# Kernel tuning notes

Hardware: AMD Instinct MI355X
Metric: run time of the kernel (lower is better)

## Reference

```python
import jax, jax.numpy as jnp
import numpy as np

DIM = 1024
HEADS = 16
HEAD_DIM = DIM // HEADS
DECAY = 0.95
EPS = 1e-5


def setup_inputs() -> dict:
    key = jax.random.key(0)
    ks = jax.random.split(key, 11)
    B, S, D = 2, 2048, DIM
    s = 1.0 / np.sqrt(D)
    inp = {
        'x': jax.random.normal(ks[0], (B, S, D), dtype=jnp.float32),
        'Wq': jax.random.normal(ks[1], (D, D), dtype=jnp.float32) * s,
        'bq': jnp.zeros((D,), jnp.float32),
        'Wk': jax.random.normal(ks[2], (D, D), dtype=jnp.float32) * s,
        'bk': jnp.zeros((D,), jnp.float32),
        'Wv': jax.random.normal(ks[3], (D, D), dtype=jnp.float32) * s,
        'bv': jnp.zeros((D,), jnp.float32),
        'Wo': jax.random.normal(ks[4], (D, D), dtype=jnp.float32) * s,
        'bo': jnp.zeros((D,), jnp.float32),
        'gamma': jnp.ones((D,), jnp.float32),
        'beta': jnp.zeros((D,), jnp.float32),
    }
    return inp


def _decay_mask(S, dtype):
    idx = jnp.arange(S)
    diff = (idx[:, None] - idx[None, :]).astype(jnp.float32)
    # decay^(i-j) for i >= j, else 0
    mask = jnp.where(diff >= 0, jnp.exp(diff * np.log(DECAY)), 0.0)
    return mask.astype(dtype)


def reference(x, Wq, bq, Wk, bk, Wv, bv, Wo, bo, gamma, beta):
    B, S, D = x.shape
    H, hd = HEADS, HEAD_DIM

    def split_heads(y):  # [B,S,D] -> [B,H,S,hd]
        return y.reshape(B, S, H, hd).transpose(0, 2, 1, 3)

    q = split_heads(x @ Wq + bq)
    k = split_heads(x @ Wk + bk)
    v = split_heads(x @ Wv + bv)

    mask = _decay_mask(S, x.dtype)  # [S,S]
    scores = jnp.einsum('bhid,bhjd->bhij', q, k) * mask
    out = jnp.einsum('bhij,bhjd->bhid', scores, v)  # [B,H,S,hd]

    out = out.transpose(0, 2, 1, 3).reshape(B, S, D)
    out = out @ Wo + bo

    # GroupNorm(H groups) applied over channel dim with seq as spatial dim
    y = out.transpose(0, 2, 1)            # [B,D,S]
    yg = y.reshape(B, H, hd, S)
    mu = yg.mean(axis=(2, 3), keepdims=True)
    var = yg.var(axis=(2, 3), keepdims=True)
    yn = (yg - mu) / jnp.sqrt(var + EPS)
    yn = yn.reshape(B, D, S) * gamma[None, :, None] + beta[None, :, None]
    return yn.transpose(0, 2, 1)          # [B,S,D]
```

## Files before the change

kernel.cpp:

```cpp
#include <hip/hip_runtime.h>
#include <hip/hip_bf16.h>

typedef unsigned short u16;
typedef __attribute__((ext_vector_type(8))) short short8;
typedef __attribute__((ext_vector_type(4))) float f32x4;
typedef __attribute__((ext_vector_type(4))) unsigned short u16x4;

#define SEQ 2048
#define NH 16
#define HD 64
#define DM 1024
#define LN_DECAY (-0.051293294387550536f)
#define WIN_TILES 4

__device__ __forceinline__ float b2f(u16 u) {
    return __uint_as_float(((unsigned int)u) << 16);
}
__device__ __forceinline__ u16 f2b(float f) {
    unsigned int u = __float_as_uint(f);
    u += 0x7fffu + ((u >> 16) & 1u);
    return (u16)(u >> 16);
}
__device__ __forceinline__ f32x4 mfma16(short8 a, short8 b, f32x4 c) {
    return __builtin_amdgcn_mfma_f32_16x16x32_bf16(a, b, c, 0, 0, 0);
}
__device__ __forceinline__ void gld_lds16(const u16* g, u16* l) {
    __builtin_amdgcn_global_load_lds(
        (const __attribute__((address_space(1))) void*)g,
        (__attribute__((address_space(3))) void*)l, 16, 0, 0);
}

__global__ __launch_bounds__(64) void detect_dtype(const u16* __restrict__ W,
                                                   int* __restrict__ flag) {
    int t = threadIdx.x;
    int hit = 0;
    for (int i = t; i < 512; i += 64) {
        u16 u = W[2 * i];
        int e = (u >> 7) & 0xFF;
        if (e >= 0xC0) hit = 1;
    }
    unsigned long long m = __ballot(hit);
    if (t == 0) *flag = (m != 0ULL) ? 1 : 0;
}

__global__ __launch_bounds__(256) void convert_x(const void* __restrict__ x,
                                                 const int* __restrict__ flag,
                                                 u16* __restrict__ xc) {
    int i = (blockIdx.x * 256 + threadIdx.x) * 4;
    if (*flag) {
        f32x4 v = *(const f32x4*)((const float*)x + i);
        u16x4 o = { f2b(v[0]), f2b(v[1]), f2b(v[2]), f2b(v[3]) };
        *(u16x4*)(xc + i) = o;
    } else {
        *(u16x4*)(xc + i) = *(const u16x4*)((const u16*)x + i);
    }
}

__global__ __launch_bounds__(256) void convert_small(
    const void* __restrict__ p0, const void* __restrict__ p1,
    const void* __restrict__ p2, const void* __restrict__ p3,
    const void* __restrict__ p4, const void* __restrict__ p5,
    const int* __restrict__ flag,
    u16* __restrict__ o0, u16* __restrict__ o1, u16* __restrict__ o2,
    u16* __restrict__ o3, u16* __restrict__ o4, u16* __restrict__ o5) {
    const void* in; u16* out;
    switch (blockIdx.x) {
        case 0: in = p0; out = o0; break;
        case 1: in = p1; out = o1; break;
        case 2: in = p2; out = o2; break;
        case 3: in = p3; out = o3; break;
        case 4: in = p4; out = o4; break;
        default: in = p5; out = o5; break;
    }
    int i = threadIdx.x * 4;
    if (*flag) {
        f32x4 v = *(const f32x4*)((const float*)in + i);
        u16x4 o = { f2b(v[0]), f2b(v[1]), f2b(v[2]), f2b(v[3]) };
        *(u16x4*)(out + i) = o;
    } else {
        *(u16x4*)(out + i) = *(const u16x4*)((const u16*)in + i);
    }
}

__global__ __launch_bounds__(256) void transpose4(
    const void* __restrict__ W0, const void* __restrict__ W1,
    const void* __restrict__ W2, const void* __restrict__ W3,
    const int* __restrict__ flag,
    u16* __restrict__ T0, u16* __restrict__ T1,
    u16* __restrict__ T2, u16* __restrict__ T3)
{
    __shared__ u16 tile[32][33];
    const void* W; u16* T;
    int z = blockIdx.z;
    if (z == 0)      { W = W0; T = T0; }
    else if (z == 1) { W = W1; T = T1; }
    else if (z == 2) { W = W2; T = T2; }
    else             { W = W3; T = T3; }
    int fl = *flag;
    int t = threadIdx.x;
    int r = t >> 5, c = t & 31;
    int bn = blockIdx.x * 32, bk = blockIdx.y * 32;
#pragma unroll
    for (int i = 0; i < 4; i++) {
        size_t idx = (size_t)(bk + r + i*8) * DM + bn + c;
        tile[r + i*8][c] = fl ? f2b(((const float*)W)[idx]) : ((const u16*)W)[idx];
    }
    __syncthreads();
#pragma unroll
    for (int i = 0; i < 4; i++)
        T[(size_t)(bn + r + i*8) * DM + bk + c] = tile[c][r + i*8];
}

__device__ __forceinline__ void gemm_body(
    const u16* __restrict__ A, const u16* __restrict__ BT,
    const u16* __restrict__ bias, u16* __restrict__ outB,
    float* __restrict__ outF, int mode,
    int m0, int n0, int t)
{
    __shared__ u16 As[128*32];
    __shared__ u16 Bs[128*32];
    int w = t >> 6, l = t & 63;
    int lane16 = l & 15, quad = l >> 4;
    int wm = (w >> 1) * 64, wn = (w & 1) * 64;

    int srow   = t >> 2;
    int schunk = (t & 3) ^ ((t >> 3) & 3);

    f32x4 zero = {0.f, 0.f, 0.f, 0.f};
    f32x4 acc[4][4];
#pragma unroll
    for (int i = 0; i < 4; i++)
#pragma unroll
        for (int j = 0; j < 4; j++)
            acc[i][j] = zero;

    const u16* a0 = A  + (size_t)(m0 + srow)      * DM + schunk*8;
    const u16* a1 = A  + (size_t)(m0 + srow + 64) * DM + schunk*8;
    const u16* b0 = BT + (size_t)(n0 + srow)      * DM + schunk*8;
    const u16* b1 = BT + (size_t)(n0 + srow + 64) * DM + schunk*8;

    for (int k0 = 0; k0 < DM; k0 += 32) {
        __syncthreads();
        gld_lds16(a0 + k0, &As[t*8]);
        gld_lds16(a1 + k0, &As[2048 + t*8]);
        gld_lds16(b0 + k0, &Bs[t*8]);
        gld_lds16(b1 + k0, &Bs[2048 + t*8]);
        __syncthreads();
        short8 af[4], bf[4];
#pragma unroll
        for (int i = 0; i < 4; i++) {
            int ra = wm + i*16 + lane16;
            int rb = wn + i*16 + lane16;
            af[i] = *(const short8*)(&As[ra*32 + ((quad ^ ((ra>>1)&3))*8)]);
            bf[i] = *(const short8*)(&Bs[rb*32 + ((quad ^ ((rb>>1)&3))*8)]);
        }
#pragma unroll
        for (int i = 0; i < 4; i++)
#pragma unroll
            for (int j = 0; j < 4; j++)
                acc[i][j] = mfma16(af[i], bf[j], acc[i][j]);
    }

#pragma unroll
    for (int i = 0; i < 4; i++) {
#pragma unroll
        for (int j = 0; j < 4; j++) {
            int n = n0 + wn + j*16 + lane16;
            float bv = b2f(bias[n]);
#pragma unroll
            for (int r = 0; r < 4; r++) {
                int m = m0 + wm + i*16 + quad*4 + r;
                float v = acc[i][j][r] + bv;
                if (mode == 3) {
                    outF[(size_t)m*DM + n] = v;
                } else {
                    int b = m >> 11, s = m & (SEQ-1);
                    int h = n >> 6,  d = n & (HD-1);
                    if (mode == 2)
                        outB[(((size_t)(b*NH + h))*HD + d)*SEQ + s] = f2b(v);
                    else
                        outB[(((size_t)(b*NH + h))*SEQ + s)*HD + d] = f2b(v);
                }
            }
        }
    }
}

__global__ __launch_bounds__(256) void gemm_qkv(
    const u16* __restrict__ x,
    const u16* __restrict__ WqT, const u16* __restrict__ WkT, const u16* __restrict__ WvT,
    const u16* __restrict__ bq, const u16* __restrict__ bk, const u16* __restrict__ bv,
    u16* __restrict__ qb, u16* __restrict__ kb, u16* __restrict__ vTb)
{
    int z = blockIdx.z;
    const u16* BT   = (z==0) ? WqT : (z==1) ? WkT : WvT;
    const u16* bias = (z==0) ? bq  : (z==1) ? bk  : bv;
    u16* outB       = (z==0) ? qb  : (z==1) ? kb  : vTb;
    gemm_body(x, BT, bias, outB, nullptr, (z==2) ? 2 : 0,
              blockIdx.x * 128, blockIdx.y * 128, threadIdx.x);
}

__global__ __launch_bounds__(256) void gemm_out(
    const u16* __restrict__ attn, const u16* __restrict__ WoT,
    const u16* __restrict__ bo, float* __restrict__ proj)
{
    gemm_body(attn, WoT, bo, nullptr, proj, 3,
              blockIdx.x * 128, blockIdx.y * 128, threadIdx.x);
}

__global__ __launch_bounds__(256) void retention(
    const u16* __restrict__ q, const u16* __restrict__ k,
    const u16* __restrict__ vT, u16* __restrict__ attn)
{
    __shared__ u16 Ks[64*64];
    __shared__ u16 Vs[64*64];
    __shared__ u16 Ps[4][16*64];

    int qt = blockIdx.x, bh = blockIdx.y;
    int t = threadIdx.x, w = t >> 6, l = t & 63;
    int c = l & 15, qd = l >> 4;
    int qbase = qt * 64;
    int iwave = qbase + w*16;

    const u16* qh = q  + (size_t)bh * SEQ * HD;
    const u16* kh = k  + (size_t)bh * SEQ * HD;
    const u16* vh = vT + (size_t)bh * HD * SEQ;

    float D[4], E[4];
#pragma unroll
    for (int r = 0; r < 4; r++)
        D[r] = __expf((float)(qd*4 + r) * LN_DECAY);
#pragma unroll
    for (int st = 0; st < 4; st++)
        E[st] = __expf(-(float)(st*16 + c) * LN_DECAY);

    int sr = t >> 3, sc8 = t & 7;

    short8 qf[2];
#pragma unroll
    for (int kk = 0; kk < 2; kk++)
        qf[kk] = *(const short8*)(qh + (size_t)(iwave + c)*HD + kk*32 + qd*8);

    f32x4 zero = {0.f, 0.f, 0.f, 0.f};
    f32x4 oacc[4] = {zero, zero, zero, zero};

    int jt0 = (qt > WIN_TILES) ? (qt - WIN_TILES) : 0;
#pragma unroll 1
    for (int jt = jt0; jt <= qt; jt++) {
        int jbase = jt * 64;
        __syncthreads();
        {
            int r0 = sr, r1 = sr + 32;
            *(short8*)(&Ks[r0*64 + ((sc8 ^ (r0&7))*8)]) = *(const short8*)(kh + (size_t)(jbase+r0)*HD + sc8*8);
            *(short8*)(&Ks[r1*64 + ((sc8 ^ (r1&7))*8)]) = *(const short8*)(kh + (size_t)(jbase+r1)*HD + sc8*8);
            *(short8*)(&Vs[r0*64 + ((sc8 ^ (r0&7))*8)]) = *(const short8*)(vh + (size_t)r0*SEQ + jbase + sc8*8);
            *(short8*)(&Vs[r1*64 + ((sc8 ^ (r1&7))*8)]) = *(const short8*)(vh + (size_t)(r1)*SEQ + jbase + sc8*8);
        }
        __syncthreads();

        f32x4 sacc[4] = {zero, zero, zero, zero};
#pragma unroll
        for (int kk = 0; kk < 2; kk++) {
#pragma unroll
            for (int st = 0; st < 4; st++) {
                int row = st*16 + c;
                short8 bf = *(const short8*)(&Ks[row*64 + (((kk*4+qd) ^ (row&7))*8)]);
                sacc[st] = mfma16(qf[kk], bf, sacc[st]);
            }
        }

        float base = __expf((float)(iwave - jbase) * LN_DECAY);
#pragma unroll
        for (int st = 0; st < 4; st++) {
            int j = jbase + st*16 + c;
            float bE = base * E[st];
#pragma unroll
            for (int r = 0; r < 4; r++) {
                int i = iwave + qd*4 + r;
                float val = (i >= j) ? sacc[st][r] * (bE * D[r]) : 0.0f;
                int row = qd*4 + r;
                int col = st*16 + c;
                Ps[w][row*64 + (((col>>3) ^ (row&7))*8) + (col&7)] = f2b(val);
            }
        }
        asm volatile("s_waitcnt lgkmcnt(0)" ::: "memory");
        short8 pf[2];
#pragma unroll
        for (int kk = 0; kk < 2; kk++)
            pf[kk] = *(const short8*)(&Ps[w][c*64 + (((kk*4+qd) ^ (c&7))*8)]);

#pragma unroll
        for (int kk = 0; kk < 2; kk++) {
#pragma unroll
            for (int nt = 0; nt < 4; nt++) {
                int row = nt*16 + c;
                short8 vf = *(const short8*)(&Vs[row*64 + (((kk*4+qd) ^ (row&7))*8)]);
                oacc[nt] = mfma16(pf[kk], vf, oacc[nt]);
            }
        }
    }

    int b = bh >> 4, h = bh & (NH-1);
#pragma unroll
    for (int nt = 0; nt < 4; nt++) {
        int d = h*HD + nt*16 + c;
#pragma unroll
        for (int r = 0; r < 4; r++) {
            int s = iwave + qd*4 + r;
            attn[((size_t)(b*SEQ + s))*DM + d] = f2b(oacc[nt][r]);
        }
    }
}

__global__ __launch_bounds__(256) void gn_partial(
    const float* __restrict__ proj, float* __restrict__ partials)
{
    int bg = blockIdx.x;
    int chunk = blockIdx.y;
    int b = bg >> 4, g = bg & (NH-1);
    const float* base = proj + (size_t)b*SEQ*DM + g*HD;
    int tid = threadIdx.x;
    int rlane = tid & 15;
    int rrow  = tid >> 4;
    float s = 0.f, ss = 0.f;
#pragma unroll
    for (int it = 0; it < 8; it++) {
        int srow = chunk*128 + it*16 + rrow;
        f32x4 v = *(const f32x4*)(base + (size_t)srow*DM + rlane*4);
        s  += v[0] + v[1] + v[2] + v[3];
        ss += v[0]*v[0] + v[1]*v[1] + v[2]*v[2] + v[3]*v[3];
    }
#pragma unroll
    for (int off = 32; off > 0; off >>= 1) {
        s  += __shfl_down(s, off);
        ss += __shfl_down(ss, off);
    }
    __shared__ float red[8];
    int w = tid >> 6, l = tid & 63;
    if (l == 0) { red[w*2] = s; red[w*2+1] = ss; }
    __syncthreads();
    if (tid == 0) {
        float S  = red[0]+red[2]+red[4]+red[6];
        float SS = red[1]+red[3]+red[5]+red[7];
        partials[(bg*16 + chunk)*2]     = S;
        partials[(bg*16 + chunk)*2 + 1] = SS;
    }
}

__global__ __launch_bounds__(64) void gn_finalize(
    const float* __restrict__ partials, float* __restrict__ stats)
{
    int bg = blockIdx.x;
    int l = threadIdx.x;
    float s  = (l < 16) ? partials[(bg*16 + l)*2]     : 0.f;
    float ss = (l < 16) ? partials[(bg*16 + l)*2 + 1] : 0.f;
#pragma unroll
    for (int off = 8; off > 0; off >>= 1) {
        s  += __shfl_down(s, off);
        ss += __shfl_down(ss, off);
    }
    if (l == 0) {
        const float inv = 1.0f / (float)(SEQ*HD);
        float mu = s * inv;
        float var = ss * inv - mu*mu;
        stats[bg*2]   = mu;
        stats[bg*2+1] = rsqrtf(var + 1e-5f);
    }
}

__global__ __launch_bounds__(256) void gn_apply(
    const float* __restrict__ proj, const float* __restrict__ stats,
    const u16* __restrict__ gamma, const u16* __restrict__ beta,
    const int* __restrict__ flag, void* __restrict__ outv)
{
    int idx = blockIdx.x * 256 + threadIdx.x;
    int d = idx & (DM-1);
    int bs = idx >> 10;
    int b = bs >> 11;
    int g = d >> 6;
    float mu   = stats[(b*NH + g)*2];
    float rstd = stats[(b*NH + g)*2 + 1];
    float v = (proj[idx] - mu) * rstd * b2f(gamma[d]) + b2f(beta[d]);
    if (*flag) ((float*)outv)[idx] = v;
    else       ((u16*)outv)[idx]   = f2b(v);
}

extern "C" void kernel_launch(void* const* d_in, const int* in_sizes, int n_in,
                              void* d_out, int out_size, void* d_ws, size_t ws_size,
                              hipStream_t stream) {
    const void* x     = d_in[0];
    const void* Wq    = d_in[1];
    const void* bq    = d_in[2];
    const void* Wk    = d_in[3];
    const void* bk    = d_in[4];
    const void* Wv    = d_in[5];
    const void* bv    = d_in[6];
    const void* Wo    = d_in[7];
    const void* bo    = d_in[8];
    const void* gamma = d_in[9];
    const void* beta  = d_in[10];

    const size_t MB = 1024*1024;
    char* ws = (char*)d_ws;
    int*   flag     = (int*)ws;
    u16*   bqc      = (u16*)(ws + 4096);
    u16*   bkc      = (u16*)(ws + 8192);
    u16*   bvc      = (u16*)(ws + 12288);
    u16*   boc      = (u16*)(ws + 16384);
    u16*   gammac   = (u16*)(ws + 20480);
    u16*   betac    = (u16*)(ws + 24576);
    float* stats    = (float*)(ws + 28672);
    float* partials = (float*)(ws + 32768);
    u16*   xc     = (u16*)(ws + 1*MB);
    u16*   WqT    = (u16*)(ws + 9*MB);
    u16*   WkT    = (u16*)(ws + 11*MB);
    u16*   WvT    = (u16*)(ws + 13*MB);
    u16*   WoT    = (u16*)(ws + 15*MB);
    u16*   qb     = (u16*)(ws + 17*MB);
    u16*   kb     = (u16*)(ws + 25*MB);
    u16*   vTb    = (u16*)(ws + 33*MB);
    u16*   attn   = (u16*)(ws + 41*MB);
    float* proj   = (float*)(ws + 17*MB);

    detect_dtype<<<1, 64, 0, stream>>>((const u16*)Wq, flag);
    convert_x<<<4096, 256, 0, stream>>>(x, flag, xc);
    convert_small<<<6, 256, 0, stream>>>(bq, bk, bv, bo, gamma, beta, flag,
                                         bqc, bkc, bvc, boc, gammac, betac);
    transpose4<<<dim3(32, 32, 4), 256, 0, stream>>>(Wq, Wk, Wv, Wo, flag, WqT, WkT, WvT, WoT);
    gemm_qkv<<<dim3(32, 8, 3), 256, 0, stream>>>(xc, WqT, WkT, WvT, bqc, bkc, bvc, qb, kb, vTb);
    retention<<<dim3(32, 32), 256, 0, stream>>>(qb, kb, vTb, attn);
    gemm_out<<<dim3(32, 8), 256, 0, stream>>>(attn, WoT, boc, proj);
    gn_partial<<<dim3(32, 16), 256, 0, stream>>>(proj, partials);
    gn_finalize<<<32, 64, 0, stream>>>(partials, stats);
    gn_apply<<<(SEQ*DM*2)/256, 256, 0, stream>>>(proj, stats, gammac, betac, flag, d_out);
}
```

Measured before the change: 193.9 us.

## Fuse prep kernels and GroupNorm statistics into GEMM epilogue via atomics

```diff
diff --git a/kernel.cpp b/kernel.cpp
--- a/kernel.cpp
+++ b/kernel.cpp
@@ -29,92 +29,83 @@
         (const __attribute__((address_space(1))) void*)g,
         (__attribute__((address_space(3))) void*)l, 16, 0, 0);
 }
-
-__global__ __launch_bounds__(64) void detect_dtype(const u16* __restrict__ W,
-                                                   int* __restrict__ flag) {
-    int t = threadIdx.x;
+__device__ __forceinline__ int detect_fl(const u16* Wq, int lane) {
     int hit = 0;
-    for (int i = t; i < 512; i += 64) {
-        u16 u = W[2 * i];
-        int e = (u >> 7) & 0xFF;
-        if (e >= 0xC0) hit = 1;
-    }
-    unsigned long long m = __ballot(hit);
-    if (t == 0) *flag = (m != 0ULL) ? 1 : 0;
-}
-
-__global__ __launch_bounds__(256) void convert_x(const void* __restrict__ x,
-                                                 const int* __restrict__ flag,
-                                                 u16* __restrict__ xc) {
-    int i = (blockIdx.x * 256 + threadIdx.x) * 4;
-    if (*flag) {
-        f32x4 v = *(const f32x4*)((const float*)x + i);
-        u16x4 o = { f2b(v[0]), f2b(v[1]), f2b(v[2]), f2b(v[3]) };
-        *(u16x4*)(xc + i) = o;
+#pragma unroll
+    for (int j = 0; j < 4; j++) {
+        u16 u = Wq[2*(lane + 64*j)];
+        if (((u >> 7) & 0xFF) >= 0xC0) hit = 1;
+    }
+    return (__ballot(hit) != 0ULL) ? 1 : 0;
+}
+
+__global__ __launch_bounds__(256) void prep(
+    const void* __restrict__ x,
+    const void* __restrict__ Wq, const void* __restrict__ Wk,
+    const void* __restrict__ Wv, const void* __restrict__ Wo,
+    const void* __restrict__ bq, const void* __restrict__ bk,
+    const void* __restrict__ bv, const void* __restrict__ bo,
+    const void* __restrict__ gamma, const void* __restrict__ beta,
+    u16* __restrict__ xc,
+    u16* __restrict__ WqT, u16* __restrict__ WkT,
+    u16* __restrict__ WvT, u16* __restrict__ WoT,
+    u16* __restrict__ bqc, u16* __restrict__ bkc, u16* __restrict__ bvc,
+    u16* __restrict__ boc, u16* __restrict__ gammac, u16* __restrict__ betac,
+    int* __restrict__ flag, float* __restrict__ statsAcc)
+{
+    __shared__ u16 tileS[32][33];
+    int bid = blockIdx.x, tid = threadIdx.x;
+    int fl = detect_fl((const u16*)Wq, tid & 63);
+
+    if (bid < 4096) {
+        int i = (bid*256 + tid)*4;
+        if (fl) {
+            f32x4 v = *(const f32x4*)((const float*)x + i);
+            u16x4 o = { f2b(v[0]), f2b(v[1]), f2b(v[2]), f2b(v[3]) };
+            *(u16x4*)(xc + i) = o;
+        } else {
+            *(u16x4*)(xc + i) = *(const u16x4*)((const u16*)x + i);
+        }
+    } else if (bid == 4096) {
+        const void* ins[6] = {bq, bk, bv, bo, gamma, beta};
+        u16* outs[6] = {bqc, bkc, bvc, boc, gammac, betac};
+        int i = tid*4;
+#pragma unroll
+        for (int a = 0; a < 6; a++) {
+            if (fl) {
+                f32x4 v = *(const f32x4*)((const float*)ins[a] + i);
+                u16x4 o = { f2b(v[0]), f2b(v[1]), f2b(v[2]), f2b(v[3]) };
+                *(u16x4*)(outs[a] + i) = o;
+            } else {
+                *(u16x4*)(outs[a] + i) = *(const u16x4*)((const u16*)ins[a] + i);
+            }
+        }
+        if (tid == 0) *flag = fl;
+        if (tid < 64) statsAcc[tid] = 0.f;
     } else {
-        *(u16x4*)(xc + i) = *(const u16x4*)((const u16*)x + i);
-    }
-}
-
-__global__ __launch_bounds__(256) void convert_small(
-    const void* __restrict__ p0, const void* __restrict__ p1,
-    const void* __restrict__ p2, const void* __restrict__ p3,
-    const void* __restrict__ p4, const void* __restrict__ p5,
-    const int* __restrict__ flag,
-    u16* __restrict__ o0, u16* __restrict__ o1, u16* __restrict__ o2,
-    u16* __restrict__ o3, u16* __restrict__ o4, u16* __restrict__ o5) {
-    const void* in; u16* out;
-    switch (blockIdx.x) {
-        case 0: in = p0; out = o0; break;
-        case 1: in = p1; out = o1; break;
-        case 2: in = p2; out = o2; break;
-        case 3: in = p3; out = o3; break;
-        case 4: in = p4; out = o4; break;
-        default: in = p5; out = o5; break;
-    }
-    int i = threadIdx.x * 4;
-    if (*flag) {
-        f32x4 v = *(const f32x4*)((const float*)in + i);
-        u16x4 o = { f2b(v[0]), f2b(v[1]), f2b(v[2]), f2b(v[3]) };
-        *(u16x4*)(out + i) = o;
-    } else {
-        *(u16x4*)(out + i) = *(const u16x4*)((const u16*)in + i);
-    }
-}
-
-__global__ __launch_bounds__(256) void transpose4(
-    const void* __restrict__ W0, const void* __restrict__ W1,
-    const void* __restrict__ W2, const void* __restrict__ W3,
-    const int* __restrict__ flag,
-    u16* __restrict__ T0, u16* __restrict__ T1,
-    u16* __restrict__ T2, u16* __restrict__ T3)
-{
-    __shared__ u16 tile[32][33];
-    const void* W; u16* T;
-    int z = blockIdx.z;
-    if (z == 0)      { W = W0; T = T0; }
-    else if (z == 1) { W = W1; T = T1; }
-    else if (z == 2) { W = W2; T = T2; }
-    else             { W = W3; T = T3; }
-    int fl = *flag;
-    int t = threadIdx.x;
-    int r = t >> 5, c = t & 31;
-    int bn = blockIdx.x * 32, bk = blockIdx.y * 32;
-#pragma unroll
-    for (int i = 0; i < 4; i++) {
-        size_t idx = (size_t)(bk + r + i*8) * DM + bn + c;
-        tile[r + i*8][c] = fl ? f2b(((const float*)W)[idx]) : ((const u16*)W)[idx];
-    }
-    __syncthreads();
-#pragma unroll
-    for (int i = 0; i < 4; i++)
-        T[(size_t)(bn + r + i*8) * DM + bk + c] = tile[c][r + i*8];
-}
-
+        int tb = bid - 4097;
+        int wsel = tb >> 10, tile = tb & 1023;
+        const void* W = (wsel==0) ? Wq : (wsel==1) ? Wk : (wsel==2) ? Wv : Wo;
+        u16* T        = (wsel==0) ? WqT : (wsel==1) ? WkT : (wsel==2) ? WvT : WoT;
+        int bn = (tile & 31)*32, bk_ = (tile >> 5)*32;
+        int r = tid >> 5, c = tid & 31;
+#pragma unroll
+        for (int i2 = 0; i2 < 4; i2++) {
+            size_t idx = (size_t)(bk_ + r + i2*8)*DM + bn + c;
+            tileS[r + i2*8][c] = fl ? f2b(((const float*)W)[idx]) : ((const u16*)W)[idx];
+        }
+        __syncthreads();
+#pragma unroll
+        for (int i2 = 0; i2 < 4; i2++)
+            T[(size_t)(bn + r + i2*8)*DM + bk_ + c] = tileS[c][r + i2*8];
+    }
+}
+
+template<int MODE>
 __device__ __forceinline__ void gemm_body(
     const u16* __restrict__ A, const u16* __restrict__ BT,
     const u16* __restrict__ bias, u16* __restrict__ outB,
-    float* __restrict__ outF, int mode,
+    float* __restrict__ outF, float* __restrict__ stats,
     int m0, int n0, int t)
 {
     __shared__ u16 As[128*32];
@@ -161,6 +152,7 @@
                 acc[i][j] = mfma16(af[i], bf[j], acc[i][j]);
     }
 
+    float s = 0.f, ss = 0.f;
 #pragma unroll
     for (int i = 0; i < 4; i++) {
 #pragma unroll
@@ -171,17 +163,31 @@
             for (int r = 0; r < 4; r++) {
                 int m = m0 + wm + i*16 + quad*4 + r;
                 float v = acc[i][j][r] + bv;
-                if (mode == 3) {
+                if (MODE == 3) {
                     outF[(size_t)m*DM + n] = v;
+                    s += v; ss += v*v;
                 } else {
-                    int b = m >> 11, s = m & (SEQ-1);
+                    int b = m >> 11, sq = m & (SEQ-1);
                     int h = n >> 6,  d = n & (HD-1);
-                    if (mode == 2)
-                        outB[(((size_t)(b*NH + h))*HD + d)*SEQ + s] = f2b(v);
+                    if (MODE == 2)
+                        outB[(((size_t)(b*NH + h))*HD + d)*SEQ + sq] = f2b(v);
                     else
-                        outB[(((size_t)(b*NH + h))*SEQ + s)*HD + d] = f2b(v);
+                        outB[(((size_t)(b*NH + h))*SEQ + sq)*HD + d] = f2b(v);
                 }
             }
+        }
+    }
+    if (MODE == 3) {
+#pragma unroll
+        for (int off = 32; off > 0; off >>= 1) {
+            s  += __shfl_down(s, off);
+            ss += __shfl_down(ss, off);
+        }
+        if (l == 0) {
+            int b = m0 >> 11;
+            int g = (n0 + wn) >> 6;
+            atomicAdd(&stats[(b*NH + g)*2],     s);
+            atomicAdd(&stats[(b*NH + g)*2 + 1], ss);
         }
     }
 }
@@ -196,16 +202,21 @@
     const u16* BT   = (z==0) ? WqT : (z==1) ? WkT : WvT;
     const u16* bias = (z==0) ? bq  : (z==1) ? bk  : bv;
     u16* outB       = (z==0) ? qb  : (z==1) ? kb  : vTb;
-    gemm_body(x, BT, bias, outB, nullptr, (z==2) ? 2 : 0,
-              blockIdx.x * 128, blockIdx.y * 128, threadIdx.x);
+    if (z == 2)
+        gemm_body<2>(x, BT, bias, outB, nullptr, nullptr,
+                     blockIdx.x * 128, blockIdx.y * 128, threadIdx.x);
+    else
+        gemm_body<0>(x, BT, bias, outB, nullptr, nullptr,
+                     blockIdx.x * 128, blockIdx.y * 128, threadIdx.x);
 }
 
 __global__ __launch_bounds__(256) void gemm_out(
     const u16* __restrict__ attn, const u16* __restrict__ WoT,
-    const u16* __restrict__ bo, float* __restrict__ proj)
-{
-    gemm_body(attn, WoT, bo, nullptr, proj, 3,
-              blockIdx.x * 128, blockIdx.y * 128, threadIdx.x);
+    const u16* __restrict__ bo, float* __restrict__ proj,
+    float* __restrict__ statsAcc)
+{
+    gemm_body<3>(attn, WoT, bo, nullptr, proj, statsAcc,
+                 blockIdx.x * 128, blockIdx.y * 128, threadIdx.x);
 }
 
 __global__ __launch_bounds__(256) void retention(
@@ -312,77 +323,32 @@
     }
 }
 
-__global__ __launch_bounds__(256) void gn_partial(
-    const float* __restrict__ proj, float* __restrict__ partials)
-{
-    int bg = blockIdx.x;
-    int chunk = blockIdx.y;
-    int b = bg >> 4, g = bg & (NH-1);
-    const float* base = proj + (size_t)b*SEQ*DM + g*HD;
-    int tid = threadIdx.x;
-    int rlane = tid & 15;
-    int rrow  = tid >> 4;
-    float s = 0.f, ss = 0.f;
-#pragma unroll
-    for (int it = 0; it < 8; it++) {
-        int srow = chunk*128 + it*16 + rrow;
-        f32x4 v = *(const f32x4*)(base + (size_t)srow*DM + rlane*4);
-        s  += v[0] + v[1] + v[2] + v[3];
-        ss += v[0]*v[0] + v[1]*v[1] + v[2]*v[2] + v[3]*v[3];
-    }
-#pragma unroll
-    for (int off = 32; off > 0; off >>= 1) {
-        s  += __shfl_down(s, off);
-        ss += __shfl_down(ss, off);
-    }
-    __shared__ float red[8];
-    int w = tid >> 6, l = tid & 63;
-    if (l == 0) { red[w*2] = s; red[w*2+1] = ss; }
-    __syncthreads();
-    if (tid == 0) {
-        float S  = red[0]+red[2]+red[4]+red[6];
-        float SS = red[1]+red[3]+red[5]+red[7];
-        partials[(bg*16 + chunk)*2]     = S;
-        partials[(bg*16 + chunk)*2 + 1] = SS;
-    }
-}
-
-__global__ __launch_bounds__(64) void gn_finalize(
-    const float* __restrict__ partials, float* __restrict__ stats)
-{
-    int bg = blockIdx.x;
-    int l = threadIdx.x;
-    float s  = (l < 16) ? partials[(bg*16 + l)*2]     : 0.f;
-    float ss = (l < 16) ? partials[(bg*16 + l)*2 + 1] : 0.f;
-#pragma unroll
-    for (int off = 8; off > 0; off >>= 1) {
-        s  += __shfl_down(s, off);
-        ss += __shfl_down(ss, off);
-    }
-    if (l == 0) {
-        const float inv = 1.0f / (float)(SEQ*HD);
-        float mu = s * inv;
-        float var = ss * inv - mu*mu;
-        stats[bg*2]   = mu;
-        stats[bg*2+1] = rsqrtf(var + 1e-5f);
-    }
-}
-
 __global__ __launch_bounds__(256) void gn_apply(
-    const float* __restrict__ proj, const float* __restrict__ stats,
+    const float* __restrict__ proj, const float* __restrict__ statsAcc,
     const u16* __restrict__ gamma, const u16* __restrict__ beta,
     const int* __restrict__ flag, void* __restrict__ outv)
 {
-    int idx = blockIdx.x * 256 + threadIdx.x;
-    int d = idx & (DM-1);
-    int bs = idx >> 10;
-    int b = bs >> 11;
+    int base = (blockIdx.x*256 + threadIdx.x)*4;
+    int d = base & (DM-1);
+    int b = base >> 21;
     int g = d >> 6;
-    float mu   = stats[(b*NH + g)*2];
-    float rstd = stats[(b*NH + g)*2 + 1];
-    float v = (proj[idx] - mu) * rstd * b2f(gamma[d]) + b2f(beta[d]);
-    if (*flag) ((float*)outv)[idx] = v;
-    else       ((u16*)outv)[idx]   = f2b(v);
+    float S  = statsAcc[(b*NH + g)*2];
+    float SS = statsAcc[(b*NH + g)*2 + 1];
+    const float inv = 1.0f/(float)(SEQ*HD);
+    float mu = S*inv;
+    float rstd = rsqrtf(SS*inv - mu*mu + 1e-5f);
+    f32x4 v = *(const f32x4*)(proj + base);
+    float o0 = (v[0]-mu)*rstd*b2f(gamma[d])   + b2f(beta[d]);
+    float o1 = (v[1]-mu)*rstd*b2f(gamma[d+1]) + b2f(beta[d+1]);
+    float o2 = (v[2]-mu)*rstd*b2f(gamma[d+2]) + b2f(beta[d+2]);
+    float o3 = (v[3]-mu)*rstd*b2f(gamma[d+3]) + b2f(beta[d+3]);
+    if (*flag) {
+        f32x4 ov = {o0, o1, o2, o3};
+        *(f32x4*)((float*)outv + base) = ov;
+    } else {
+        u16x4 ov = {f2b(o0), f2b(o1), f2b(o2), f2b(o3)};
+        *(u16x4*)((u16*)outv + base) = ov;
+    }
 }
 
 extern "C" void kernel_launch(void* const* d_in, const int* in_sizes, int n_in,
@@ -409,8 +375,7 @@
     u16*   boc      = (u16*)(ws + 16384);
     u16*   gammac   = (u16*)(ws + 20480);
     u16*   betac    = (u16*)(ws + 24576);
-    float* stats    = (float*)(ws + 28672);
-    float* partials = (float*)(ws + 32768);
+    float* statsAcc = (float*)(ws + 28672);
     u16*   xc     = (u16*)(ws + 1*MB);
     u16*   WqT    = (u16*)(ws + 9*MB);
     u16*   WkT    = (u16*)(ws + 11*MB);
@@ -422,15 +387,12 @@
     u16*   attn   = (u16*)(ws + 41*MB);
     float* proj   = (float*)(ws + 17*MB);
 
-    detect_dtype<<<1, 64, 0, stream>>>((const u16*)Wq, flag);
-    convert_x<<<4096, 256, 0, stream>>>(x, flag, xc);
-    convert_small<<<6, 256, 0, stream>>>(bq, bk, bv, bo, gamma, beta, flag,
-                                         bqc, bkc, bvc, boc, gammac, betac);
-    transpose4<<<dim3(32, 32, 4), 256, 0, stream>>>(Wq, Wk, Wv, Wo, flag, WqT, WkT, WvT, WoT);
+    prep<<<8193, 256, 0, stream>>>(x, Wq, Wk, Wv, Wo, bq, bk, bv, bo, gamma, beta,
+                                   xc, WqT, WkT, WvT, WoT,
+                                   bqc, bkc, bvc, boc, gammac, betac,
+                                   flag, statsAcc);
     gemm_qkv<<<dim3(32, 8, 3), 256, 0, stream>>>(xc, WqT, WkT, WvT, bqc, bkc, bvc, qb, kb, vTb);
     retention<<<dim3(32, 32), 256, 0, stream>>>(qb, kb, vTb, attn);
-    gemm_out<<<dim3(32, 8), 256, 0, stream>>>(attn, WoT, boc, proj);
-    gn_partial<<<dim3(32, 16), 256, 0, stream>>>(proj, partials);
-    gn_finalize<<<32, 64, 0, stream>>>(partials, stats);
-    gn_apply<<<(SEQ*DM*2)/256, 256, 0, stream>>>(proj, stats, gammac, betac, flag, d_out);
-}
+    gemm_out<<<dim3(32, 8), 256, 0, stream>>>(attn, WoT, boc, proj, statsAcc);
+    gn_apply<<<4096, 256, 0, stream>>>(proj, statsAcc, gammac, betac, flag, d_out);
+}
```

Result: faster. 186.1 us (-4.0%).
